# Kernel optimization log

Hardware: AMD Instinct MI355X
Metric: run time of the kernel (lower is better)

The kernel has to match this reference:

```python
import jax, jax.numpy as jnp
import numpy as np

EMB = 1024
DM = 64
NH = 16

def setup_inputs() -> dict:
    key = jax.random.key(0)
    ks = jax.random.split(key, 11)
    bs, slen = 2, 2048
    s = 1.0 / np.sqrt(EMB)
    inp = {
        'Q': jax.random.normal(ks[0], (bs, slen, EMB), jnp.float32),
        'K': jax.random.normal(ks[1], (bs, slen, EMB), jnp.float32),
        'V': jax.random.normal(ks[2], (bs, slen, EMB), jnp.float32),
        'Wq': jax.random.normal(ks[3], (EMB, DM * NH), jnp.float32) * s,
        'bq': jnp.zeros((DM * NH,), jnp.float32),
        'Wk': jax.random.normal(ks[4], (EMB, DM * NH), jnp.float32) * s,
        'bk': jnp.zeros((DM * NH,), jnp.float32),
        'Wv': jax.random.normal(ks[5], (EMB, DM * NH), jnp.float32) * s,
        'bv': jnp.zeros((DM * NH,), jnp.float32),
        'Wo': jax.random.normal(ks[6], (DM * NH, EMB), jnp.float32) * (1.0 / np.sqrt(DM * NH)),
        'bo': jnp.zeros((EMB,), jnp.float32),
    }
    return inp

def reference(Q, K, V, Wq, bq, Wk, bk, Wv, bv, Wo, bo):
    bs, q_len, _ = Q.shape
    kv_len = K.shape[1]
    scale = 1.0 / np.sqrt(DM)
    # project and split heads: (n, l, h, d)
    q = (scale * (Q @ Wq + bq)).reshape(bs, q_len, NH, DM)
    k = (K @ Wk + bk).reshape(bs, kv_len, NH, DM)
    v = (V @ Wv + bv).reshape(bs, kv_len, NH, DM)
    # scores (n, h, l, s) -- full S x S matrix, as in the original
    qk = jnp.einsum('nlhd,nshd->nhls', q, k)
    a = jax.nn.softmax(qk, axis=-1)  # dropout p=0 -> identity
    o = jnp.einsum('nhls,nshd->nlhd', a, v).reshape(bs, q_len, NH * DM)
    return o @ Wo + bo
```

## Files before the change

kernel.cpp:

```cpp
#include <hip/hip_runtime.h>
#include <cstdint>
#include <cstddef>

#define EMB  1024
#define DM   64
#define NH   16
#define SLEN 2048
#define BS   2

typedef _Float16 f16x8 __attribute__((ext_vector_type(8)));
typedef _Float16 f16x4 __attribute__((ext_vector_type(4)));
typedef __fp16   hf2   __attribute__((ext_vector_type(2)));
typedef __fp16   hf4   __attribute__((ext_vector_type(4)));
typedef __fp16   hf8   __attribute__((ext_vector_type(8)));
typedef float    f32x4 __attribute__((ext_vector_type(4)));

#define ASYNC_LD16(gp, lp)                                                        \
    __builtin_amdgcn_global_load_lds(                                             \
        (const __attribute__((address_space(1))) void*)(gp),                      \
        (__attribute__((address_space(3))) void*)(lp), 16, 0, 0)

__global__ __launch_bounds__(256)
void prep(const float* __restrict__ Q, const float* __restrict__ K,
          const float* __restrict__ V,
          const float* __restrict__ Wq, const float* __restrict__ Wk,
          const float* __restrict__ Wv, const float* __restrict__ Wo,
          _Float16* __restrict__ Qh, _Float16* __restrict__ Kh,
          _Float16* __restrict__ Vh,
          _Float16* __restrict__ WqT, _Float16* __restrict__ WkT,
          _Float16* __restrict__ WvT, _Float16* __restrict__ WoT)
{
    __shared__ float t[64][65];
    const int z = blockIdx.z;
    if (z < 3) {
        const float* in  = (z == 0) ? Q : (z == 1) ? K : V;
        _Float16*    out = (z == 0) ? Qh : (z == 1) ? Kh : Vh;
        size_t i = ((size_t)blockIdx.x * 256 + threadIdx.x) * 8;
        float4 a = *(const float4*)(in + i);
        float4 b = *(const float4*)(in + i + 4);
        f16x8 o;
        o[0] = (_Float16)a.x; o[1] = (_Float16)a.y; o[2] = (_Float16)a.z; o[3] = (_Float16)a.w;
        o[4] = (_Float16)b.x; o[5] = (_Float16)b.y; o[6] = (_Float16)b.z; o[7] = (_Float16)b.w;
        *(f16x8*)(out + i) = o;
        return;
    }
    if (blockIdx.x >= 256) return;
    const float* W;
    _Float16*    T;
    switch (z - 3) {
        case 0:  W = Wq; T = WqT; break;
        case 1:  W = Wk; T = WkT; break;
        case 2:  W = Wv; T = WvT; break;
        default: W = Wo; T = WoT; break;
    }
    const int tid = threadIdx.x;
    const int bn  = (blockIdx.x & 15) * 64;
    const int bk  = (blockIdx.x >> 4) * 64;

    #pragma unroll
    for (int p = 0; p < 4; ++p) {
        int row = p * 16 + (tid >> 4);
        int col = (tid & 15) * 4;
        float4 v = *(const float4*)(W + (size_t)(bk + row) * EMB + bn + col);
        t[row][col+0] = v.x; t[row][col+1] = v.y; t[row][col+2] = v.z; t[row][col+3] = v.w;
    }
    __syncthreads();
    #pragma unroll
    for (int p = 0; p < 4; ++p) {
        int nr = p * 16 + (tid >> 4);
        int kc = (tid & 15) * 4;
        f16x4 o;
        o[0] = (_Float16)t[kc+0][nr];
        o[1] = (_Float16)t[kc+1][nr];
        o[2] = (_Float16)t[kc+2][nr];
        o[3] = (_Float16)t[kc+3][nr];
        *(f16x4*)&T[(size_t)(bn + nr) * EMB + bk + kc] = o;
    }
}

__device__ __forceinline__
void gemm_core(const _Float16* __restrict__ A, const _Float16* __restrict__ Bt,
               const float* __restrict__ bias, float* __restrict__ Cf,
               _Float16* __restrict__ Ch, int M, int N, int K,
               float scale, int mode, int bx, int by)
{
    __shared__ __align__(16) _Float16 As[128 * 32];
    __shared__ __align__(16) _Float16 Bs[128 * 32];

    const int tid  = threadIdx.x;
    const int lane = tid & 63;
    const int wave = tid >> 6;
    const int c    = lane & 15;
    const int quad = lane >> 4;
    const int bm   = by * 128;
    const int bn   = bx * 128;
    const int wm   = (wave >> 1) * 64;
    const int wn   = (wave & 1) * 64;

    f32x4 acc[4][4];
    #pragma unroll
    for (int i = 0; i < 4; ++i)
        #pragma unroll
        for (int j = 0; j < 4; ++j)
            #pragma unroll
            for (int r = 0; r < 4; ++r) acc[i][j][r] = 0.f;

    const char* gA = (const char*)(A + (size_t)(bm + (tid >> 2)) * K) + (tid & 3) * 16;
    const char* gB = (const char*)(Bt + (size_t)(bn + (tid >> 2)) * K) + (tid & 3) * 16;
    char* lA = (char*)As + wave * 1024;
    char* lB = (char*)Bs + wave * 1024;
    const size_t rowskip = (size_t)64 * K * 2;

    for (int k0 = 0; k0 < K; k0 += 32) {
        __syncthreads();
        ASYNC_LD16(gA + (size_t)k0 * 2,           lA);
        ASYNC_LD16(gA + rowskip + (size_t)k0 * 2, lA + 4096);
        ASYNC_LD16(gB + (size_t)k0 * 2,           lB);
        ASYNC_LD16(gB + rowskip + (size_t)k0 * 2, lB + 4096);
        __syncthreads();

        f16x8 af[4], bf[4];
        #pragma unroll
        for (int i = 0; i < 4; ++i)
            af[i] = *(const f16x8*)&As[(wm + i * 16 + c) * 32 + quad * 8];
        #pragma unroll
        for (int j = 0; j < 4; ++j)
            bf[j] = *(const f16x8*)&Bs[(wn + j * 16 + c) * 32 + quad * 8];

        #pragma unroll
        for (int i = 0; i < 4; ++i)
            #pragma unroll
            for (int j = 0; j < 4; ++j)
                acc[i][j] = __builtin_amdgcn_mfma_f32_16x16x32_f16(af[i], bf[j], acc[i][j], 0, 0, 0);
    }

    float bcol[4];
    #pragma unroll
    for (int j = 0; j < 4; ++j) bcol[j] = bias[bn + wn + j * 16 + c];

    #pragma unroll
    for (int i = 0; i < 4; ++i) {
        int m0 = bm + wm + i * 16 + quad * 4;
        #pragma unroll
        for (int j = 0; j < 4; ++j) {
            int n = bn + wn + j * 16 + c;
            if (mode == 0) {
                #pragma unroll
                for (int r = 0; r < 4; ++r)
                    Cf[(size_t)(m0 + r) * N + n] = acc[i][j][r] + bcol[j];
            } else if (mode == 1) {
                int h = n >> 6, d = n & 63;
                #pragma unroll
                for (int r = 0; r < 4; ++r) {
                    int mm = m0 + r;
                    int b = mm >> 11, l = mm & (SLEN - 1);
                    Ch[(((size_t)(b * NH + h)) * SLEN + l) * DM + d] =
                        (_Float16)((acc[i][j][r] + bcol[j]) * scale);
                }
            } else {
                int h = n >> 6, d = n & 63;
                int b = m0 >> 11, l = m0 & (SLEN - 1);
                f16x4 o;
                #pragma unroll
                for (int r = 0; r < 4; ++r)
                    o[r] = (_Float16)(acc[i][j][r] + bcol[j]);
                *(f16x4*)&Ch[(((size_t)(b * NH + h)) * DM + d) * SLEN + l] = o;
            }
        }
    }
}

__global__ __launch_bounds__(256)
void gemm_qkv(const _Float16* __restrict__ Qh, const _Float16* __restrict__ Kh,
              const _Float16* __restrict__ Vh,
              const _Float16* __restrict__ WqT, const _Float16* __restrict__ WkT,
              const _Float16* __restrict__ WvT,
              const float* __restrict__ bq, const float* __restrict__ bk,
              const float* __restrict__ bv,
              _Float16* __restrict__ q_ws, _Float16* __restrict__ k_ws,
              _Float16* __restrict__ v_ws)
{
    const _Float16 *A, *Bt;
    const float* bias;
    _Float16* Ch;
    float scale;
    int mode;
    if (blockIdx.z == 0)      { A = Qh; Bt = WqT; bias = bq; Ch = q_ws; scale = 0.18033688f; mode = 1; }
    else if (blockIdx.z == 1) { A = Kh; Bt = WkT; bias = bk; Ch = k_ws; scale = 1.0f;        mode = 1; }
    else                      { A = Vh; Bt = WvT; bias = bv; Ch = v_ws; scale = 1.0f;        mode = 2; }
    gemm_core(A, Bt, bias, nullptr, Ch, BS * SLEN, NH * DM, EMB, scale, mode,
              blockIdx.x, blockIdx.y);
}

__global__ __launch_bounds__(256)
void gemm_out(const _Float16* __restrict__ Oh, const _Float16* __restrict__ WoT,
              const float* __restrict__ bo, float* __restrict__ out)
{
    gemm_core(Oh, WoT, bo, out, nullptr, BS * SLEN, EMB, NH * DM, 1.0f, 0,
              blockIdx.x, blockIdx.y);
}

__global__ __launch_bounds__(512)
void attn_mfma(const _Float16* __restrict__ qw, const _Float16* __restrict__ kw,
               const _Float16* __restrict__ vwT, _Float16* __restrict__ ow)
{
    __shared__ __align__(16) _Float16 Kt[2][64 * 64];
    __shared__ __align__(16) _Float16 Vt[2][64 * 64];

    const int tid  = threadIdx.x;
    const int lane = tid & 63;
    const int wave = tid >> 6;
    const int c    = lane & 15;
    const int quad = lane >> 4;
    const int qg   = wave & 3;
    const int kh   = wave >> 2;
    const int bh   = blockIdx.y;
    const int b    = bh >> 4;
    const int h    = bh & 15;
    const int qbase = blockIdx.x * 128 + qg * 32;

    const _Float16* kb = kw  + (size_t)bh * SLEN * DM;
    const _Float16* vb = vwT + (size_t)bh * DM * SLEN;
    const _Float16* qb = qw  + (size_t)bh * SLEN * DM;

    f16x8 qf[2][2];
    #pragma unroll
    for (int t = 0; t < 2; ++t)
        #pragma unroll
        for (int ch = 0; ch < 2; ++ch)
            qf[t][ch] = *(const f16x8*)(qb + (size_t)(qbase + t*16 + c) * DM + ch*32 + quad*8);

    f32x4 oacc[2][4];
    f32x4 lacc[2];
    #pragma unroll
    for (int t = 0; t < 2; ++t) {
        #pragma unroll
        for (int dg = 0; dg < 4; ++dg)
            #pragma unroll
            for (int r = 0; r < 4; ++r) oacc[t][dg][r] = 0.f;
        #pragma unroll
        for (int r = 0; r < 4; ++r) lacc[t][r] = 0.f;
    }

    const f16x8 ones8 = {(_Float16)1.f, (_Float16)1.f, (_Float16)1.f, (_Float16)1.f,
                         (_Float16)1.f, (_Float16)1.f, (_Float16)1.f, (_Float16)1.f};
    const f32x4 zero4 = {0.f, 0.f, 0.f, 0.f};

    const int r0  = wave * 8 + (lane >> 3);
    const int lc0 = (((lane & 7) ^ ((lane >> 3) & 7)) * 16);
    const char* gk = (const char*)kb + r0 * 128 + lc0;
    const char* gv = (const char*)vb + (size_t)r0 * 4096 + lc0;
    char* lK = (char*)&Kt[0][0] + wave * 1024;
    char* lV = (char*)&Vt[0][0] + wave * 1024;

    ASYNC_LD16(gk, lK);
    ASYNC_LD16(gv, lV);
    gk += 8192; gv += 128;
    __syncthreads();

    auto tile = [&](int cur, bool pf) {
        if (pf) {
            char* pk = (char*)&Kt[cur ^ 1][0] + wave * 1024;
            char* pv = (char*)&Vt[cur ^ 1][0] + wave * 1024;
            ASYNC_LD16(gk, pk);
            ASYNC_LD16(gv, pv);
            gk += 8192; gv += 128;
        }

        f16x8 kf[2][2];
        #pragma unroll
        for (int kg = 0; kg < 2; ++kg)
            #pragma unroll
            for (int ch = 0; ch < 2; ++ch)
                kf[kg][ch] = *(const f16x8*)
                    &Kt[cur][(kh*32 + kg*16 + c) * 64 + (((ch*4 + quad) ^ (c & 7)) * 8)];

        f32x4 s[2][2];
        #pragma unroll
        for (int t = 0; t < 2; ++t)
            #pragma unroll
            for (int kg = 0; kg < 2; ++kg) {
                s[t][kg] = __builtin_amdgcn_mfma_f32_16x16x32_f16(kf[kg][0], qf[t][0], zero4,   0, 0, 0);
                s[t][kg] = __builtin_amdgcn_mfma_f32_16x16x32_f16(kf[kg][1], qf[t][1], s[t][kg], 0, 0, 0);
            }

        f16x8 pf8[2];
        #pragma unroll
        for (int t = 0; t < 2; ++t) {
            hf4 h4[2];
            #pragma unroll
            for (int u = 0; u < 2; ++u) {
                float p0 = __builtin_amdgcn_exp2f(s[t][u][0]);
                float p1 = __builtin_amdgcn_exp2f(s[t][u][1]);
                float p2 = __builtin_amdgcn_exp2f(s[t][u][2]);
                float p3 = __builtin_amdgcn_exp2f(s[t][u][3]);
                hf2 lo = __builtin_amdgcn_cvt_pkrtz(p0, p1);
                hf2 hi = __builtin_amdgcn_cvt_pkrtz(p2, p3);
                h4[u] = __builtin_shufflevector(lo, hi, 0, 1, 2, 3);
            }
            hf8 h8 = __builtin_shufflevector(h4[0], h4[1], 0, 1, 2, 3, 4, 5, 6, 7);
            pf8[t] = __builtin_bit_cast(f16x8, h8);
        }

        #pragma unroll
        for (int t = 0; t < 2; ++t)
            lacc[t] = __builtin_amdgcn_mfma_f32_16x16x32_f16(pf8[t], ones8, lacc[t], 0, 0, 0);

        #pragma unroll
        for (int dg = 0; dg < 4; ++dg) {
            f16x4 vf[2];
            #pragma unroll
            for (int u = 0; u < 2; ++u)
                vf[u] = *(const f16x4*)
                    &Vt[cur][(dg*16 + c) * 64 +
                             (((kh*4 + 2*u + (quad >> 1)) ^ (c & 7)) * 8) + (quad & 1) * 4];
            f16x8 v8 = __builtin_shufflevector(vf[0], vf[1], 0, 1, 2, 3, 4, 5, 6, 7);
            #pragma unroll
            for (int t = 0; t < 2; ++t)
                oacc[t][dg] = __builtin_amdgcn_mfma_f32_16x16x32_f16(pf8[t], v8, oacc[t][dg], 0, 0, 0);
        }
        __syncthreads();
    };

    for (int it = 0; it < SLEN / 64 - 2; it += 2) {
        tile(0, true);
        tile(1, true);
    }
    tile(0, true);
    tile(1, false);

    float* mb = (float*)&Kt[0][0];
    #pragma unroll
    for (int t = 0; t < 2; ++t) {
        if (kh == 1) {
            float* p = mb + ((qg * 64 + lane) * 20);
            *(f32x4*)(p +  0) = oacc[t][0];
            *(f32x4*)(p +  4) = oacc[t][1];
            *(f32x4*)(p +  8) = oacc[t][2];
            *(f32x4*)(p + 12) = oacc[t][3];
            *(f32x4*)(p + 16) = lacc[t];
        }
        __syncthreads();
        if (kh == 0) {
            const float* p = mb + ((qg * 64 + lane) * 20);
            f32x4 po[4], pl;
            po[0] = *(const f32x4*)(p +  0);
            po[1] = *(const f32x4*)(p +  4);
            po[2] = *(const f32x4*)(p +  8);
            po[3] = *(const f32x4*)(p + 12);
            pl    = *(const f32x4*)(p + 16);
            #pragma unroll
            for (int r = 0; r < 4; ++r) {
                float linv = 1.0f / (lacc[t][r] + pl[r]);
                int row = qbase + t*16 + quad*4 + r;
                #pragma unroll
                for (int dg = 0; dg < 4; ++dg)
                    ow[((size_t)b * SLEN + row) * EMB + h * DM + dg*16 + c] =
                        (_Float16)((oacc[t][dg][r] + po[dg][r]) * linv);
            }
        }
        __syncthreads();
    }
}

extern "C" void kernel_launch(void* const* d_in, const int* in_sizes, int n_in,
                              void* d_out, int out_size, void* d_ws, size_t ws_size,
                              hipStream_t stream)
{
    const float* Q  = (const float*)d_in[0];
    const float* K  = (const float*)d_in[1];
    const float* V  = (const float*)d_in[2];
    const float* Wq = (const float*)d_in[3];
    const float* bq = (const float*)d_in[4];
    const float* Wk = (const float*)d_in[5];
    const float* bk = (const float*)d_in[6];
    const float* Wv = (const float*)d_in[7];
    const float* bv = (const float*)d_in[8];
    const float* Wo = (const float*)d_in[9];
    const float* bo = (const float*)d_in[10];
    float* out = (float*)d_out;

    const size_t MN = (size_t)BS * SLEN * NH * DM;
    const size_t WW = (size_t)EMB * NH * DM;

    _Float16* base = (_Float16*)d_ws;
    _Float16* Qh   = base;
    _Float16* Kh   = Qh  + MN;
    _Float16* Vh   = Kh  + MN;
    _Float16* WqT  = Vh  + MN;
    _Float16* WkT  = WqT + WW;
    _Float16* WvT  = WkT + WW;
    _Float16* WoT  = WvT + WW;
    _Float16* q_ws = WoT + WW;
    _Float16* k_ws = q_ws + MN;
    _Float16* v_ws = k_ws + MN;
    _Float16* o_ws = v_ws + MN;

    dim3 blk(256);

    prep<<<dim3(2048, 1, 7), blk, 0, stream>>>(Q, K, V, Wq, Wk, Wv, Wo,
                                               Qh, Kh, Vh, WqT, WkT, WvT, WoT);

    gemm_qkv<<<dim3(8, 32, 3), blk, 0, stream>>>(Qh, Kh, Vh, WqT, WkT, WvT,
                                                 bq, bk, bv, q_ws, k_ws, v_ws);

    attn_mfma<<<dim3(SLEN / 128, BS * NH), dim3(512), 0, stream>>>(q_ws, k_ws, v_ws, o_ws);

    gemm_out<<<dim3(8, 32, 1), blk, 0, stream>>>(o_ws, WoT, bo, out);
}
```

Measured before the change: 224.8 us.

## Load K/V fragments directly from global memory into registers in attention

Removes the LDS double-buffered K/V staging and its per-tile barriers from the attention kernel. Each wave now loads its K and V MFMA fragments straight from global memory, with K prefetched one tile ahead in registers. LDS is kept only for the final merge of the two key halves, and launch bounds now request higher occupancy. In exchange, every wave issues its own global loads, so there is no sharing across waves and the loads are less coalesced, and the occupancy hint may force register spills.

```diff
diff --git a/kernel.cpp b/kernel.cpp
--- a/kernel.cpp
+++ b/kernel.cpp
@@ -200,12 +200,11 @@
               blockIdx.x, blockIdx.y);
 }
 
-__global__ __launch_bounds__(512)
+__global__ __launch_bounds__(512, 4)
 void attn_mfma(const _Float16* __restrict__ qw, const _Float16* __restrict__ kw,
                const _Float16* __restrict__ vwT, _Float16* __restrict__ ow)
 {
-    __shared__ __align__(16) _Float16 Kt[2][64 * 64];
-    __shared__ __align__(16) _Float16 Vt[2][64 * 64];
+    __shared__ __align__(16) float mrg[4 * 64 * 20];
 
     const int tid  = threadIdx.x;
     const int lane = tid & 63;
@@ -246,94 +245,76 @@
                          (_Float16)1.f, (_Float16)1.f, (_Float16)1.f, (_Float16)1.f};
     const f32x4 zero4 = {0.f, 0.f, 0.f, 0.f};
 
-    const int r0  = wave * 8 + (lane >> 3);
-    const int lc0 = (((lane & 7) ^ ((lane >> 3) & 7)) * 16);
-    const char* gk = (const char*)kb + r0 * 128 + lc0;
-    const char* gv = (const char*)vb + (size_t)r0 * 4096 + lc0;
-    char* lK = (char*)&Kt[0][0] + wave * 1024;
-    char* lV = (char*)&Vt[0][0] + wave * 1024;
-
-    ASYNC_LD16(gk, lK);
-    ASYNC_LD16(gv, lV);
-    gk += 8192; gv += 128;
-    __syncthreads();
-
-    auto tile = [&](int cur, bool pf) {
-        if (pf) {
-            char* pk = (char*)&Kt[cur ^ 1][0] + wave * 1024;
-            char* pv = (char*)&Vt[cur ^ 1][0] + wave * 1024;
-            ASYNC_LD16(gk, pk);
-            ASYNC_LD16(gv, pv);
-            gk += 8192; gv += 128;
-        }
-
-        f16x8 kf[2][2];
+    const _Float16* kp = kb + (size_t)(kh*32 + c) * DM + quad*8;
+    const _Float16* vp = vb + (size_t)c * SLEN + kh*32 + quad*4;
+
+    const int NT = SLEN / 64;
+
+    f16x8 kfA[2][2], kfB[2][2];
+    #pragma unroll
+    for (int kg = 0; kg < 2; ++kg)
+        #pragma unroll
+        for (int ch = 0; ch < 2; ++ch)
+            kfA[kg][ch] = *(const f16x8*)(kp + (size_t)(kg*16) * DM + ch*32);
+
+    auto body = [&](int tt, f16x8 (&kc)[2][2], f16x8 (&kn)[2][2]) {
+        f16x4 vf4[4][2];
+        #pragma unroll
+        for (int dg = 0; dg < 4; ++dg)
+            #pragma unroll
+            for (int u = 0; u < 2; ++u)
+                vf4[dg][u] = *(const f16x4*)(vp + (size_t)dg * 16 * SLEN + tt*64 + u*16);
+
+        const int tn = (tt + 1 < NT) ? tt + 1 : tt;
         #pragma unroll
         for (int kg = 0; kg < 2; ++kg)
             #pragma unroll
             for (int ch = 0; ch < 2; ++ch)
-                kf[kg][ch] = *(const f16x8*)
-                    &Kt[cur][(kh*32 + kg*16 + c) * 64 + (((ch*4 + quad) ^ (c & 7)) * 8)];
-
-        f32x4 s[2][2];
-        #pragma unroll
-        for (int t = 0; t < 2; ++t)
+                kn[kg][ch] = *(const f16x8*)(kp + (size_t)(tn*64 + kg*16) * DM + ch*32);
+
+        f16x8 pf8[2];
+        #pragma unroll
+        for (int t = 0; t < 2; ++t) {
+            f32x4 s[2];
             #pragma unroll
             for (int kg = 0; kg < 2; ++kg) {
-                s[t][kg] = __builtin_amdgcn_mfma_f32_16x16x32_f16(kf[kg][0], qf[t][0], zero4,   0, 0, 0);
-                s[t][kg] = __builtin_amdgcn_mfma_f32_16x16x32_f16(kf[kg][1], qf[t][1], s[t][kg], 0, 0, 0);
+                s[kg] = __builtin_amdgcn_mfma_f32_16x16x32_f16(kc[kg][0], qf[t][0], zero4, 0, 0, 0);
+                s[kg] = __builtin_amdgcn_mfma_f32_16x16x32_f16(kc[kg][1], qf[t][1], s[kg], 0, 0, 0);
             }
-
-        f16x8 pf8[2];
-        #pragma unroll
-        for (int t = 0; t < 2; ++t) {
             hf4 h4[2];
             #pragma unroll
             for (int u = 0; u < 2; ++u) {
-                float p0 = __builtin_amdgcn_exp2f(s[t][u][0]);
-                float p1 = __builtin_amdgcn_exp2f(s[t][u][1]);
-                float p2 = __builtin_amdgcn_exp2f(s[t][u][2]);
-                float p3 = __builtin_amdgcn_exp2f(s[t][u][3]);
+                float p0 = __builtin_amdgcn_exp2f(s[u][0]);
+                float p1 = __builtin_amdgcn_exp2f(s[u][1]);
+                float p2 = __builtin_amdgcn_exp2f(s[u][2]);
+                float p3 = __builtin_amdgcn_exp2f(s[u][3]);
                 hf2 lo = __builtin_amdgcn_cvt_pkrtz(p0, p1);
                 hf2 hi = __builtin_amdgcn_cvt_pkrtz(p2, p3);
                 h4[u] = __builtin_shufflevector(lo, hi, 0, 1, 2, 3);
             }
             hf8 h8 = __builtin_shufflevector(h4[0], h4[1], 0, 1, 2, 3, 4, 5, 6, 7);
             pf8[t] = __builtin_bit_cast(f16x8, h8);
-        }
-
-        #pragma unroll
-        for (int t = 0; t < 2; ++t)
             lacc[t] = __builtin_amdgcn_mfma_f32_16x16x32_f16(pf8[t], ones8, lacc[t], 0, 0, 0);
+        }
 
         #pragma unroll
         for (int dg = 0; dg < 4; ++dg) {
-            f16x4 vf[2];
-            #pragma unroll
-            for (int u = 0; u < 2; ++u)
-                vf[u] = *(const f16x4*)
-                    &Vt[cur][(dg*16 + c) * 64 +
-                             (((kh*4 + 2*u + (quad >> 1)) ^ (c & 7)) * 8) + (quad & 1) * 4];
-            f16x8 v8 = __builtin_shufflevector(vf[0], vf[1], 0, 1, 2, 3, 4, 5, 6, 7);
+            f16x8 v8 = __builtin_shufflevector(vf4[dg][0], vf4[dg][1], 0, 1, 2, 3, 4, 5, 6, 7);
             #pragma unroll
             for (int t = 0; t < 2; ++t)
                 oacc[t][dg] = __builtin_amdgcn_mfma_f32_16x16x32_f16(pf8[t], v8, oacc[t][dg], 0, 0, 0);
         }
-        __syncthreads();
     };
 
-    for (int it = 0; it < SLEN / 64 - 2; it += 2) {
-        tile(0, true);
-        tile(1, true);
-    }
-    tile(0, true);
-    tile(1, false);
-
-    float* mb = (float*)&Kt[0][0];
+    for (int it = 0; it < NT; it += 2) {
+        body(it,     kfA, kfB);
+        body(it + 1, kfB, kfA);
+    }
+
     #pragma unroll
     for (int t = 0; t < 2; ++t) {
         if (kh == 1) {
-            float* p = mb + ((qg * 64 + lane) * 20);
+            float* p = mrg + ((qg * 64 + lane) * 20);
             *(f32x4*)(p +  0) = oacc[t][0];
             *(f32x4*)(p +  4) = oacc[t][1];
             *(f32x4*)(p +  8) = oacc[t][2];
@@ -342,7 +323,7 @@
         }
         __syncthreads();
         if (kh == 0) {
-            const float* p = mb + ((qg * 64 + lane) * 20);
+            const float* p = mrg + ((qg * 64 + lane) * 20);
             f32x4 po[4], pl;
             po[0] = *(const f32x4*)(p +  0);
             po[1] = *(const f32x4*)(p +  4);
```

New measurement: 353.2 us. 1.57x slower.
